# Performance work log

Hardware: AMD Instinct MI355X
Metric: run time of the kernel (lower is better)

## Reference

```python
import jax, jax.numpy as jnp
import numpy as np

_PHI = (1.0 + 5.0 ** 0.5) / 2.0
_VS = np.array([[0, 1, _PHI], [0, 1, -_PHI], [0, -1, _PHI], [0, -1, -_PHI],
                [1, _PHI, 0], [1, -_PHI, 0], [-1, _PHI, 0], [-1, -_PHI, 0],
                [_PHI, 0, 1], [_PHI, 0, -1], [-_PHI, 0, 1], [-_PHI, 0, -1]], dtype=np.float32)
_VS = _VS / np.linalg.norm(_VS, axis=-1, keepdims=True)  # 12 icosahedron vertices
_COLOR_COM = np.array([(0, 1, 2, 3, 4, 5), (0, 5, 4, 3, 2, 1), (2, 5, 4, 1, 0, 3), (5, 0, 1, 3, 2, 4),
                       (3, 5, 2, 0, 4, 1), (4, 0, 5, 2, 1, 3), (1, 3, 4, 2, 0, 5), (1, 0, 2, 4, 3, 5),
                       (4, 1, 2, 5, 0, 3), (3, 1, 4, 0, 2, 5), (5, 1, 0, 4, 2, 3), (2, 4, 5, 3, 0, 1)])
_INV = np.argsort(_COLOR_COM, axis=-1)  # inverse perms: scatter_(-1, color_com, W) == gather with _INV
_C2V = np.array([(0, 1), (6, 7), (2, 11), (4, 9), (5, 8), (3, 10)])
_ROLL = np.array([(0, 1, 2, 3, 4, 5), (0, 2, 3, 4, 5, 1), (0, 3, 4, 5, 1, 2), (0, 4, 5, 1, 2, 3), (0, 5, 1, 2, 3, 4)])
_HEADS = 8


def _build_sym(Wp):
    """(..., 18) raw params -> (..., 13, 12, 6) symmetry-expanded weights."""
    lead = Wp.shape[:-1]
    top = jnp.concatenate([Wp[..., 0:1], jnp.repeat(Wp[..., 1:2], 5, axis=-1)], axis=-1)[..., None, :]
    bot = jnp.concatenate([Wp[..., 2:3], jnp.repeat(Wp[..., 3:4], 5, axis=-1)], axis=-1)[..., None, :]
    cen = jnp.concatenate([Wp[..., 4:5], jnp.repeat(Wp[..., 5:6], 5, axis=-1)], axis=-1)[..., None, :]
    sym = Wp[..., 6:18].reshape(lead + (2, 6))[..., _ROLL].reshape(lead + (10, 6))
    W13 = jnp.concatenate([top, bot, sym, cen], axis=-2)  # (..., 13, 6)
    return W13[..., _INV]  # (..., 13, 12, 6): rotated copies via inverse color permutations


def setup_inputs() -> dict:
    key = jax.random.key(0)
    ks = jax.random.split(key, 6)
    bs, V, n, di, do = 1, 2048, 16, 32, 64
    s = 0.05
    return {
        "neighbor_index": jax.random.randint(ks[0], (bs, V, n), 0, V),
        "vertices": jax.random.normal(ks[1], (bs, V, 3), dtype=jnp.float32),
        "feature_map": jax.random.normal(ks[2], (bs, di, V, 6), dtype=jnp.float32),
        "W_dim": jax.random.normal(ks[3], (di + 1, di), dtype=jnp.float32) * s,
        "W": jax.random.normal(ks[4], (do, di, 18), dtype=jnp.float32) * s,
        "W_dir": jax.random.normal(ks[5], (di * _HEADS, 18), dtype=jnp.float32) * s,
    }


def reference(neighbor_index, vertices, feature_map, W_dim, W, W_dir):
    bs, V, n = neighbor_index.shape
    do, di, _ = W.shape
    H = _HEADS
    dph = di // H
    vs = jnp.asarray(_VS)
    c2v = jnp.asarray(_C2V)
    # neighbor direction (normalized)
    neigh = jax.vmap(lambda v, idx: v[idx])(vertices, neighbor_index)  # (bs,V,n,3)
    nd = neigh - vertices[:, :, None, :]
    ndn = nd / jnp.maximum(jnp.linalg.norm(nd, axis=-1, keepdims=True), 1e-12)
    # symmetry-expanded weights
    W_ro = _build_sym(W)       # (do, di, 13, 12, 6)
    Wd_ro = _build_sym(W_dir)  # (di*H, 13, 12, 6)
    # gather neighbor features: (bs, di, V, n, 6)
    nf = jax.vmap(lambda fm, idx: fm[:, idx])(feature_map, neighbor_index)
    # direction features discretized onto the 6 color axes
    de = jnp.einsum('vi,bqni->bqnv', vs, ndn)          # (bs,V,n,12)
    de = de[..., c2v].max(axis=-1)                      # (bs,V,n,6)
    cross = jnp.concatenate([nf, de[:, None]], axis=1)  # (bs, di+1, V, n, 6)
    cross = jnp.einsum('co,bcpni->bopni', W_dim, cross)  # (bs, di, V, n, 6)
    # per-head attention over neighbors
    Wdr = Wd_ro.reshape(H, di, 13, 12, 6).transpose(0, 1, 2, 4, 3)  # (h, c, k, i, r)
    act = jnp.einsum('hckir,bcpni->hbkpnr', Wdr[:, :, :12], cross) / (dph ** 0.5)
    act = jax.nn.softmax(act, axis=-2)                  # softmax over neighbors n
    cross_h = cross.reshape(bs, H, dph, V, n, 6)
    nfm = jnp.einsum('hbkpnr,bhcpni->bhckpir', act, cross_h).reshape(bs, di, 12, V, 6, 12)
    feat = jnp.einsum('dckri,bckpir->bdkpr', W_ro[:, :, :12], nfm)   # (bs,do,12,V,12)
    center = jnp.einsum('dcri,bcpi->bdpr', W_ro[:, :, 12], feature_map)  # (bs,do,V,12)
    ka = feat.sum(axis=2) + center                       # (bs,do,V,12)
    ka = ka[..., c2v].max(axis=-1)                       # (bs,do,V,6)
    return (ka, feature_map)
```

## Files before the change

kernel.cpp:

```cpp
#include <hip/hip_runtime.h>
#include <cstdint>
#include <cstddef>

#define NN 16
#define DI 32
#define DO 64

typedef short bf16x8 __attribute__((ext_vector_type(8)));
typedef short bf16x4 __attribute__((ext_vector_type(4)));
typedef float f32x4 __attribute__((ext_vector_type(4)));

#if defined(__has_builtin)
#  if __has_builtin(__builtin_amdgcn_mfma_f32_16x16x16_bf16)
#    define MFMA_K16(a, b, c) __builtin_amdgcn_mfma_f32_16x16x16_bf16(a, b, c, 0, 0, 0)
#    define HAVE_K16 1
#  elif __has_builtin(__builtin_amdgcn_mfma_f32_16x16x16bf16_1k)
#    define MFMA_K16(a, b, c) __builtin_amdgcn_mfma_f32_16x16x16bf16_1k(a, b, c, 0, 0, 0)
#    define HAVE_K16 1
#  endif
#  if __has_builtin(__builtin_amdgcn_cvt_pk_bf16_f32)
#    define HAVE_PKBF 1
#  endif
#endif

__device__ __constant__ int c_INV[12][6] = {
  {0,1,2,3,4,5},{0,5,4,3,2,1},{4,3,0,5,2,1},{1,2,4,3,5,0},
  {3,5,2,0,4,1},{1,4,3,5,0,2},{4,0,3,1,2,5},{1,0,2,4,3,5},
  {4,1,2,5,0,3},{3,1,4,0,2,5},{2,1,4,5,3,0},{4,5,0,3,1,2}};
__device__ __constant__ int c_ROLL[5][6] = {
  {0,1,2,3,4,5},{0,2,3,4,5,1},{0,3,4,5,1,2},{0,4,5,1,2,3},{0,5,1,2,3,4}};
__device__ __constant__ float c_VS[12][3] = {
  {0.f, 0.5257311121f, 0.8506508084f},
  {0.f, 0.5257311121f, -0.8506508084f},
  {0.f, -0.5257311121f, 0.8506508084f},
  {0.f, -0.5257311121f, -0.8506508084f},
  {0.5257311121f, 0.8506508084f, 0.f},
  {0.5257311121f, -0.8506508084f, 0.f},
  {-0.5257311121f, 0.8506508084f, 0.f},
  {-0.5257311121f, -0.8506508084f, 0.f},
  {0.8506508084f, 0.f, 0.5257311121f},
  {0.8506508084f, 0.f, -0.5257311121f},
  {-0.8506508084f, 0.f, 0.5257311121f},
  {-0.8506508084f, 0.f, -0.5257311121f}};
__device__ __constant__ int c_C2V[6][2] = {{0,1},{6,7},{2,11},{4,9},{5,8},{3,10}};

__device__ inline unsigned short f2bf(float f) {
  unsigned int u = __float_as_uint(f);
  unsigned int r = (u + 0x7fffu + ((u >> 16) & 1u)) >> 16;
  return (unsigned short)r;
}
__device__ inline unsigned int pk2(float a, float b) {
#ifdef HAVE_PKBF
  typedef __bf16 bf16v2 __attribute__((ext_vector_type(2)));
  union { bf16v2 v; unsigned int u; } cv;
  cv.v = __builtin_amdgcn_cvt_pk_bf16_f32(a, b);
  return cv.u;
#else
  return (unsigned int)f2bf(a) | ((unsigned int)f2bf(b) << 16);
#endif
}
__device__ inline unsigned short f2bf_fast(float a) {
  return (unsigned short)(pk2(a, a) & 0xffffu);
}

__device__ inline float sym13(const float* __restrict__ w, int k, int j) {
  if (k == 0)  return w[j == 0 ? 0 : 1];
  if (k == 1)  return w[j == 0 ? 2 : 3];
  if (k == 12) return w[j == 0 ? 4 : 5];
  int a = (k - 2) / 5, rr = (k - 2) % 5;
  return w[6 + a * 6 + c_ROLL[rr][j]];
}

__global__ __launch_bounds__(256) void k0_expand(
    const float* __restrict__ W, const float* __restrict__ Wdir,
    const float* __restrict__ fm, const float* __restrict__ Wdim,
    unsigned short* __restrict__ A_bf,
    unsigned short* __restrict__ W2k,
    unsigned short* __restrict__ Wck,
    unsigned short* __restrict__ fmTbf,
    unsigned short* __restrict__ wdB,
    float* __restrict__ out_fm, int V) {
  int idx = blockIdx.x * 256 + threadIdx.x;
  if (idx < 221184) {
    int row = idx / 192, ci = idx % 192;
    int h = row / 144, k = (row / 12) % 12, r = row % 12;
    int c = ci / 6, i = ci % 6;
    int rt = row >> 4, rl = row & 15;
    int ks = ci >> 5, q = (ci >> 3) & 3, j = ci & 7;
    A_bf[(((rt * 6 + ks) * 4 + q) * 16 + rl) * 8 + j] =
        f2bf_fast(0.5f * sym13(&Wdir[(h * 32 + c) * 18], k, c_INV[r][i]));
  } else if (idx < 1990656) {
    int e = idx - 221184;
    int kr = e / 12288, rem = e % 12288;
    int k = kr / 12, r = kr % 12, d = rem / 192, ci = rem % 192;
    int c = ci / 6, i = ci % 6;
    int ks = ci >> 5, q = (ci >> 3) & 3, j = ci & 7;
    W2k[kr * 12288 + ((ks * 4 + q) * 64 + d) * 8 + j] =
        f2bf_fast(sym13(&W[(d * 32 + c) * 18], k, c_INV[r][i]));
  } else if (idx < 2138112) {
    int e = idx - 1990656;
    int r = e / 12288, rem = e % 12288, d = rem / 192, ci = rem % 192;
    int c = ci / 6, i = ci % 6;
    int ks = ci >> 5, q = (ci >> 3) & 3, j = ci & 7;
    Wck[r * 12288 + ((ks * 4 + q) * 64 + d) * 8 + j] =
        f2bf_fast(sym13(&W[(d * 32 + c) * 18], 12, c_INV[r][i]));
  } else if (idx < 2138112 + 192 * V) {
    int e = idx - 2138112;
    int p = e / 192, ci = e % 192, c = ci / 6, i = ci % 6;
    float v = fm[(c * V + p) * 6 + i];
    fmTbf[e] = f2bf_fast(v);
    out_fm[(c * V + p) * 6 + i] = v;
  } else {
    int e = idx - (2138112 + 192 * V);
    if (e < 2048) {
      int j = e & 7, lane = (e >> 3) & 63, kc = (e >> 9) & 1, ot = e >> 10;
      int k = kc * 32 + (lane >> 4) * 8 + j;
      int o = ot * 16 + (lane & 15);
      wdB[e] = (k <= 32) ? f2bf_fast(Wdim[k * 32 + o]) : (unsigned short)0;
    }
  }
}

__global__ __launch_bounds__(256) void k1_cross(
    const int* __restrict__ nbi, const float* __restrict__ verts,
    const float* __restrict__ fm, const unsigned short* __restrict__ wdB,
    unsigned short* __restrict__ cross_n,
    unsigned short* __restrict__ crossT_g, int V) {
  __shared__ __align__(16) unsigned short in_bf[4][96][64];
  int t = threadIdx.x, w = t >> 6, lane = t & 63;
  int quad = lane >> 4, col = lane & 15;
  int p = blockIdx.x * 4 + w;
  unsigned short* mybuf = &in_bf[w][0][0];

  for (int z = lane; z < 384; z += 64) {
    int m = z >> 2, q = z & 3;
    *(uint4*)&mybuf[m * 64 + 32 + q * 8] = make_uint4(0u, 0u, 0u, 0u);
  }

  float px = verts[p * 3 + 0], py = verts[p * 3 + 1], pz = verts[p * 3 + 2];
  for (int idx = lane; idx < 528; idx += 64) {
    int n = idx / 33, c = idx - n * 33;
    int nb = nbi[p * 16 + n];
    if (c < 32) {
      const float* src = fm + ((size_t)c * V + nb) * 6;
      float2 a  = *(const float2*)(src + 0);
      float2 b  = *(const float2*)(src + 2);
      float2 cd = *(const float2*)(src + 4);
      unsigned short* dst = &mybuf[(n * 6) * 64 + c];
      dst[0 * 64] = f2bf_fast(a.x);
      dst[1 * 64] = f2bf_fast(a.y);
      dst[2 * 64] = f2bf_fast(b.x);
      dst[3 * 64] = f2bf_fast(b.y);
      dst[4 * 64] = f2bf_fast(cd.x);
      dst[5 * 64] = f2bf_fast(cd.y);
    } else {
      float qx = verts[nb * 3 + 0] - px;
      float qy = verts[nb * 3 + 1] - py;
      float qz = verts[nb * 3 + 2] - pz;
      float L = sqrtf(qx * qx + qy * qy + qz * qz);
      float inv = 1.0f / fmaxf(L, 1e-12f);
      qx *= inv; qy *= inv; qz *= inv;
      float de[12];
      #pragma unroll
      for (int v = 0; v < 12; ++v)
        de[v] = c_VS[v][0] * qx + c_VS[v][1] * qy + c_VS[v][2] * qz;
      #pragma unroll
      for (int j = 0; j < 6; ++j)
        mybuf[(n * 6 + j) * 64 + 32] = f2bf_fast(fmaxf(de[c_C2V[j][0]], de[c_C2V[j][1]]));
    }
  }

  bf16x8 Bf[2][2];
  #pragma unroll
  for (int ot = 0; ot < 2; ++ot)
    #pragma unroll
    for (int kc = 0; kc < 2; ++kc)
      Bf[ot][kc] = *(const bf16x8*)(wdB + (size_t)((ot * 2 + kc) * 64 + lane) * 8);

  asm volatile("s_waitcnt lgkmcnt(0)" ::: "memory");

  f32x4 D[6][2];
  #pragma unroll
  for (int mt = 0; mt < 6; ++mt) {
    bf16x8 a0 = *(const bf16x8*)&mybuf[(mt * 16 + col) * 64 + quad * 8];
    bf16x8 a1 = *(const bf16x8*)&mybuf[(mt * 16 + col) * 64 + 32 + quad * 8];
    #pragma unroll
    for (int ot = 0; ot < 2; ++ot) {
      f32x4 acc = (f32x4){0.f, 0.f, 0.f, 0.f};
      acc = __builtin_amdgcn_mfma_f32_16x16x32_bf16(a0, Bf[ot][0], acc, 0, 0, 0);
      acc = __builtin_amdgcn_mfma_f32_16x16x32_bf16(a1, Bf[ot][1], acc, 0, 0, 0);
      D[mt][ot] = acc;
    }
  }

  asm volatile("s_waitcnt lgkmcnt(0)" ::: "memory");
  unsigned short* crossL = mybuf;
  #pragma unroll
  for (int mt = 0; mt < 6; ++mt) {
    #pragma unroll
    for (int ot = 0; ot < 2; ++ot) {
      #pragma unroll
      for (int r = 0; r < 4; ++r) {
        int m = mt * 16 + quad * 4 + r;
        int n = m / 6, i = m - n * 6;
        int ci = (ot * 16 + col) * 6 + i;
        crossL[ci * 16 + n] = f2bf_fast(D[mt][ot][r]);
      }
    }
  }
  asm volatile("s_waitcnt lgkmcnt(0)" ::: "memory");

  {
    uint4* ct = (uint4*)(crossT_g + (size_t)p * 3072);
    const uint4* cl4 = (const uint4*)crossL;
    for (int q = lane; q < 384; q += 64) ct[q] = cl4[q];
  }
  {
    uint4* cn = (uint4*)(cross_n + (size_t)p * 3072);
    for (int q = lane; q < 384; q += 64) {
      int n = (q * 8) / 192, ci0 = (q * 8) % 192;
      unsigned int u[4];
      #pragma unroll
      for (int h2 = 0; h2 < 4; ++h2) {
        unsigned int lo = crossL[(ci0 + 2 * h2 + 0) * 16 + n];
        unsigned int hi = crossL[(ci0 + 2 * h2 + 1) * 16 + n];
        u[h2] = lo | (hi << 16);
      }
      cn[q] = make_uint4(u[0], u[1], u[2], u[3]);
    }
  }
}

__global__ __launch_bounds__(512, 4) void k2_main(
    const unsigned short* __restrict__ A_bf,
    const unsigned short* __restrict__ cross_n,
    const unsigned short* __restrict__ crossT_g,
    unsigned short* __restrict__ nfm, int V) {
#ifdef HAVE_K16
  __shared__ __align__(16) unsigned short crossT[4][192][16];
#else
  __shared__ __align__(16) unsigned short crossT[4][192][40];
#endif
  int t = threadIdx.x;
  int w = t >> 6, lane = t & 63;
  int quad = lane >> 4, col = lane & 15;
  int p0 = blockIdx.x * 4;
  int pw = w & 1, tw = w >> 1;

  bf16x8 Afr[2][6];
  #pragma unroll
  for (int pi = 0; pi < 2; ++pi)
    #pragma unroll
    for (int ks = 0; ks < 6; ++ks)
      Afr[pi][ks] = *(const bf16x8*)(cross_n + (size_t)(p0 + pw * 2 + pi) * 3072 +
                                     col * 192 + ks * 32 + quad * 8);

#ifdef HAVE_K16
  for (int idx = t; idx < 1536; idx += 512) {
    *(uint4*)&((unsigned short*)crossT)[idx * 8] =
        *(const uint4*)(crossT_g + (size_t)p0 * 3072 + idx * 8);
  }
#else
  for (int idx = t; idx < 1536; idx += 512) {
    int p = idx / 384, rem = idx % 384, ci = rem >> 1, half = rem & 1;
    *(uint4*)&crossT[p][ci][half * 8] =
        *(const uint4*)(crossT_g + (size_t)(p0 + p) * 3072 + ci * 16 + half * 8);
  }
  for (int idx = t; idx < 1536; idx += 512) {
    int p = idx / 384, rem = idx % 384, ci = rem >> 1, half = rem & 1;
    *(uint4*)&crossT[p][ci][16 + half * 8] = make_uint4(0u, 0u, 0u, 0u);
  }
#endif
  __syncthreads();

#ifndef HAVE_K16
  int s0l = quad * 32 + col;
  int s1l = s0l + 16;
#endif

  for (int rt = tw; rt < 72; rt += 4) {
    int h = rt / 9;
    f32x4 acc[2];
    acc[0] = (f32x4){0.f, 0.f, 0.f, 0.f};
    acc[1] = (f32x4){0.f, 0.f, 0.f, 0.f};
    const unsigned short* Abase = A_bf + rt * 3072 + quad * 128 + col * 8;
    #pragma unroll
    for (int ks = 0; ks < 6; ++ks) {
      bf16x8 wf = *(const bf16x8*)(Abase + ks * 512);
      acc[0] = __builtin_amdgcn_mfma_f32_16x16x32_bf16(Afr[0][ks], wf, acc[0], 0, 0, 0);
      acc[1] = __builtin_amdgcn_mfma_f32_16x16x32_bf16(Afr[1][ks], wf, acc[1], 0, 0, 0);
    }
    int row0 = h * 24 + col;
    int row1 = min(h * 24 + 16 + col, 191);
    #pragma unroll
    for (int pi = 0; pi < 2; ++pi) {
      int p_i = pw * 2 + pi;
      float v0 = acc[pi][0], v1 = acc[pi][1], v2 = acc[pi][2], v3 = acc[pi][3];
      float mx = fmaxf(fmaxf(v0, v1), fmaxf(v2, v3));
      mx = fmaxf(mx, __shfl_xor(mx, 16));
      mx = fmaxf(mx, __shfl_xor(mx, 32));
      float e0 = __expf(v0 - mx), e1 = __expf(v1 - mx);
      float e2 = __expf(v2 - mx), e3 = __expf(v3 - mx);
      float s = (e0 + e1) + (e2 + e3);
      s += __shfl_xor(s, 16);
      s += __shfl_xor(s, 32);
      float inv = __builtin_amdgcn_rcpf(s);
      unsigned int lo = pk2(e0 * inv, e1 * inv);
      unsigned int hi = pk2(e2 * inv, e3 * inv);
      f32x4 o0 = (f32x4){0.f, 0.f, 0.f, 0.f}, o1 = o0;
#ifdef HAVE_K16
      union { uint2 u; bf16x4 v; } bcvt;
      bcvt.u = make_uint2(lo, hi);
      bf16x4 a0 = *(const bf16x4*)&crossT[p_i][row0][quad * 4];
      bf16x4 a1 = *(const bf16x4*)&crossT[p_i][row1][quad * 4];
      o0 = MFMA_K16(a0, bcvt.v, o0);
      o1 = MFMA_K16(a1, bcvt.v, o1);
#else
      unsigned int b0 = (unsigned int)__shfl((int)lo, s0l);
      unsigned int b1 = (unsigned int)__shfl((int)hi, s0l);
      unsigned int b2 = (unsigned int)__shfl((int)lo, s1l);
      unsigned int b3 = (unsigned int)__shfl((int)hi, s1l);
      bool vq = (quad < 2);
      union { uint4 u; bf16x8 v; } cvt;
      cvt.u = make_uint4(vq ? b0 : 0u, vq ? b1 : 0u, vq ? b2 : 0u, vq ? b3 : 0u);
      bf16x8 a0 = *(const bf16x8*)&crossT[p_i][row0][quad * 8];
      bf16x8 a1 = *(const bf16x8*)&crossT[p_i][row1][quad * 8];
      o0 = __builtin_amdgcn_mfma_f32_16x16x32_bf16(a0, cvt.v, o0, 0, 0, 0);
      o1 = __builtin_amdgcn_mfma_f32_16x16x32_bf16(a1, cvt.v, o1, 0, 0, 0);
#endif
      size_t rowbase = (size_t)blockIdx.x * 110592 + (size_t)(rt * 16 + col) * 96 + p_i * 24;
      uint2 w0;
      w0.x = pk2(o0[0], o0[1]);
      w0.y = pk2(o0[2], o0[3]);
      *(uint2*)(nfm + rowbase + quad * 4) = w0;
      if (quad < 2) {
        uint2 w1;
        w1.x = pk2(o1[0], o1[1]);
        w1.y = pk2(o1[2], o1[3]);
        *(uint2*)(nfm + rowbase + 16 + quad * 4) = w1;
      }
    }
  }
}

__global__ __launch_bounds__(512) void k3_feat(
    const unsigned short* __restrict__ W2k,
    const unsigned short* __restrict__ Wck,
    const unsigned short* __restrict__ fmTbf,
    const unsigned short* __restrict__ nfm,
    float* __restrict__ out, int V) {
  __shared__ float red[2][3][32][64];
  int pb = blockIdx.x, j = blockIdx.y;
  int t = threadIdx.x, w = t >> 6, lane = t & 63;
  int rhalf = w >> 2, kw = w & 3;
  int r = c_C2V[j][rhalf];
  int quad = lane >> 4, col = lane & 15;
  int p0 = pb * 32;
  f32x4 acc[4][2];
  #pragma unroll
  for (int m = 0; m < 4; ++m)
    #pragma unroll
    for (int jj = 0; jj < 2; ++jj) acc[m][jj] = (f32x4){0.f, 0.f, 0.f, 0.f};

  int base24[6];
  #pragma unroll
  for (int ks = 0; ks < 6; ++ks) {
    int ci = ks * 32 + quad * 8;
    int hh = ci / 24, oo = ci - hh * 24;
    base24[ks] = hh * 13824 + oo;
  }

  int pA = p0 + col, pB = p0 + 16 + col;
  const unsigned short* Bn0 = nfm + (size_t)(pA >> 2) * 110592 + (pA & 3) * 24;
  const unsigned short* Bn1 = nfm + (size_t)(pB >> 2) * 110592 + (pB & 3) * 24;
  const unsigned short* Bc0 = fmTbf + (size_t)pA * 192;
  const unsigned short* Bc1 = fmTbf + (size_t)pB * 192;

  int nkb = (kw == 3) ? 4 : 3;
  for (int i = 0; i < nkb; ++i) {
    int kb = kw * 3 + i;
    const unsigned short* Ab;
    int kr96 = 0;
    if (kb < 12) { Ab = W2k + (size_t)(kb * 12 + r) * 12288; kr96 = (kb * 12 + r) * 96; }
    else         { Ab = Wck + (size_t)r * 12288; }
    const unsigned short* Albase = Ab + quad * 512 + col * 8;
    #pragma unroll
    for (int ks = 0; ks < 6; ++ks) {
      bf16x8 b0, b1;
      if (kb < 12) {
        b0 = *(const bf16x8*)(Bn0 + base24[ks] + kr96);
        b1 = *(const bf16x8*)(Bn1 + base24[ks] + kr96);
      } else {
        int ko = ks * 32 + quad * 8;
        b0 = *(const bf16x8*)(Bc0 + ko);
        b1 = *(const bf16x8*)(Bc1 + ko);
      }
      #pragma unroll
      for (int m = 0; m < 4; ++m) {
        bf16x8 a = *(const bf16x8*)(Albase + ks * 2048 + m * 128);
        acc[m][0] = __builtin_amdgcn_mfma_f32_16x16x32_bf16(a, b0, acc[m][0], 0, 0, 0);
        acc[m][1] = __builtin_amdgcn_mfma_f32_16x16x32_bf16(a, b1, acc[m][1], 0, 0, 0);
      }
    }
  }
  if (kw > 0) {
    #pragma unroll
    for (int m = 0; m < 4; ++m)
      #pragma unroll
      for (int jj = 0; jj < 2; ++jj)
        #pragma unroll
        for (int rr = 0; rr < 4; ++rr)
          red[rhalf][kw - 1][m * 8 + jj * 4 + rr][lane] = acc[m][jj][rr];
  }
  __syncthreads();
  if (kw == 0) {
    #pragma unroll
    for (int m = 0; m < 4; ++m)
      #pragma unroll
      for (int jj = 0; jj < 2; ++jj)
        #pragma unroll
        for (int rr = 0; rr < 4; ++rr) {
          int ri = m * 8 + jj * 4 + rr;
          acc[m][jj][rr] += red[rhalf][0][ri][lane] + red[rhalf][1][ri][lane] + red[rhalf][2][ri][lane];
        }
  }
  if (w == 4) {
    #pragma unroll
    for (int m = 0; m < 4; ++m)
      #pragma unroll
      for (int jj = 0; jj < 2; ++jj)
        #pragma unroll
        for (int rr = 0; rr < 4; ++rr)
          red[1][0][m * 8 + jj * 4 + rr][lane] = acc[m][jj][rr];
  }
  __syncthreads();
  if (w == 0) {
    #pragma unroll
    for (int m = 0; m < 4; ++m)
      #pragma unroll
      for (int jj = 0; jj < 2; ++jj)
        #pragma unroll
        for (int rr = 0; rr < 4; ++rr) {
          float v = fmaxf(acc[m][jj][rr], red[1][0][m * 8 + jj * 4 + rr][lane]);
          int d = m * 16 + quad * 4 + rr;
          int p = p0 + jj * 16 + col;
          out[((size_t)d * V + p) * 6 + j] = v;
        }
  }
}

extern "C" void kernel_launch(void* const* d_in, const int* in_sizes, int n_in,
                              void* d_out, int out_size, void* d_ws, size_t ws_size,
                              hipStream_t stream) {
  const int* nbi = (const int*)d_in[0];
  const float* verts = (const float*)d_in[1];
  const float* fm = (const float*)d_in[2];
  const float* Wdim = (const float*)d_in[3];
  const float* W = (const float*)d_in[4];
  const float* Wdir = (const float*)d_in[5];
  float* out = (float*)d_out;
  float* ws = (float*)d_ws;
  int V = in_sizes[0] / NN;

  unsigned short* A_bf  = (unsigned short*)ws;
  unsigned short* W2k   = (unsigned short*)(ws + 110592);
  unsigned short* Wck   = (unsigned short*)(ws + 995328);
  unsigned short* fmTbf = (unsigned short*)(ws + 1069056);
  size_t o = 1069056 + (size_t)96 * V;
  unsigned short* cross_n = (unsigned short*)(ws + o);
  o += (size_t)1536 * V;
  unsigned short* crossT_g = (unsigned short*)(ws + o);
  o += (size_t)1536 * V;
  unsigned short* nfm = (unsigned short*)(ws + o);
  o += (size_t)13824 * V;
  unsigned short* wdB = (unsigned short*)(ws + o);

  int n0 = 2138112 + 192 * V + 2048;
  k0_expand<<<(n0 + 255) / 256, 256, 0, stream>>>(W, Wdir, fm, Wdim, A_bf, W2k, Wck, fmTbf,
                                                  wdB, out + (size_t)DO * V * 6, V);
  k1_cross<<<V / 4, 256, 0, stream>>>(nbi, verts, fm, wdB, cross_n, crossT_g, V);
  k2_main<<<V / 4, 512, 0, stream>>>(A_bf, cross_n, crossT_g, nfm, V);
  k3_feat<<<dim3(V / 32, 6), 512, 0, stream>>>(W2k, Wck, fmTbf, nfm, out, V);
}
```

Before: 178.7 us.

## Fuse cross-feature and attention kernels, keeping cross tile in shared memory

Merges the cross-feature kernel and the attention kernel into one launch. Each 256-thread block now handles 2 vertices, and the cross tile stays in LDS, so the cross_n and crossT global round trips go away. The direction feature term is added as a scalar FMA in fp32 instead of being padded into a second K=32 MFMA, which halves the Wdim fragment. In exchange, only 2 of the 4 waves do the cross MFMA while the rest idle. Fragments are gathered element by element from LDS, and the nfm layout changes to 2 vertices per block.

```diff
diff --git a/kernel.cpp b/kernel.cpp
--- a/kernel.cpp
+++ b/kernel.cpp
@@ -112,173 +112,114 @@
     out_fm[(c * V + p) * 6 + i] = v;
   } else {
     int e = idx - (2138112 + 192 * V);
-    if (e < 2048) {
-      int j = e & 7, lane = (e >> 3) & 63, kc = (e >> 9) & 1, ot = e >> 10;
-      int k = kc * 32 + (lane >> 4) * 8 + j;
+    if (e < 1024) {
+      int j = e & 7, lane = (e >> 3) & 63, ot = e >> 9;
+      int k = ((lane >> 4) & 3) * 8 + j;
       int o = ot * 16 + (lane & 15);
-      wdB[e] = (k <= 32) ? f2bf_fast(Wdim[k * 32 + o]) : (unsigned short)0;
-    }
-  }
-}
-
-__global__ __launch_bounds__(256) void k1_cross(
+      wdB[e] = f2bf_fast(Wdim[k * 32 + o]);
+    }
+  }
+}
+
+__global__ __launch_bounds__(256, 4) void k12_main(
     const int* __restrict__ nbi, const float* __restrict__ verts,
-    const float* __restrict__ fm, const unsigned short* __restrict__ wdB,
-    unsigned short* __restrict__ cross_n,
-    unsigned short* __restrict__ crossT_g, int V) {
-  __shared__ __align__(16) unsigned short in_bf[4][96][64];
-  int t = threadIdx.x, w = t >> 6, lane = t & 63;
-  int quad = lane >> 4, col = lane & 15;
-  int p = blockIdx.x * 4 + w;
-  unsigned short* mybuf = &in_bf[w][0][0];
-
-  for (int z = lane; z < 384; z += 64) {
-    int m = z >> 2, q = z & 3;
-    *(uint4*)&mybuf[m * 64 + 32 + q * 8] = make_uint4(0u, 0u, 0u, 0u);
-  }
-
-  float px = verts[p * 3 + 0], py = verts[p * 3 + 1], pz = verts[p * 3 + 2];
-  for (int idx = lane; idx < 528; idx += 64) {
-    int n = idx / 33, c = idx - n * 33;
-    int nb = nbi[p * 16 + n];
-    if (c < 32) {
-      const float* src = fm + ((size_t)c * V + nb) * 6;
-      float2 a  = *(const float2*)(src + 0);
-      float2 b  = *(const float2*)(src + 2);
-      float2 cd = *(const float2*)(src + 4);
-      unsigned short* dst = &mybuf[(n * 6) * 64 + c];
-      dst[0 * 64] = f2bf_fast(a.x);
-      dst[1 * 64] = f2bf_fast(a.y);
-      dst[2 * 64] = f2bf_fast(b.x);
-      dst[3 * 64] = f2bf_fast(b.y);
-      dst[4 * 64] = f2bf_fast(cd.x);
-      dst[5 * 64] = f2bf_fast(cd.y);
-    } else {
-      float qx = verts[nb * 3 + 0] - px;
-      float qy = verts[nb * 3 + 1] - py;
-      float qz = verts[nb * 3 + 2] - pz;
-      float L = sqrtf(qx * qx + qy * qy + qz * qz);
-      float inv = 1.0f / fmaxf(L, 1e-12f);
-      qx *= inv; qy *= inv; qz *= inv;
-      float de[12];
-      #pragma unroll
-      for (int v = 0; v < 12; ++v)
-        de[v] = c_VS[v][0] * qx + c_VS[v][1] * qy + c_VS[v][2] * qz;
-      #pragma unroll
-      for (int j = 0; j < 6; ++j)
-        mybuf[(n * 6 + j) * 64 + 32] = f2bf_fast(fmaxf(de[c_C2V[j][0]], de[c_C2V[j][1]]));
-    }
-  }
-
-  bf16x8 Bf[2][2];
-  #pragma unroll
-  for (int ot = 0; ot < 2; ++ot)
-    #pragma unroll
-    for (int kc = 0; kc < 2; ++kc)
-      Bf[ot][kc] = *(const bf16x8*)(wdB + (size_t)((ot * 2 + kc) * 64 + lane) * 8);
-
-  asm volatile("s_waitcnt lgkmcnt(0)" ::: "memory");
-
-  f32x4 D[6][2];
-  #pragma unroll
-  for (int mt = 0; mt < 6; ++mt) {
-    bf16x8 a0 = *(const bf16x8*)&mybuf[(mt * 16 + col) * 64 + quad * 8];
-    bf16x8 a1 = *(const bf16x8*)&mybuf[(mt * 16 + col) * 64 + 32 + quad * 8];
-    #pragma unroll
-    for (int ot = 0; ot < 2; ++ot) {
-      f32x4 acc = (f32x4){0.f, 0.f, 0.f, 0.f};
-      acc = __builtin_amdgcn_mfma_f32_16x16x32_bf16(a0, Bf[ot][0], acc, 0, 0, 0);
-      acc = __builtin_amdgcn_mfma_f32_16x16x32_bf16(a1, Bf[ot][1], acc, 0, 0, 0);
-      D[mt][ot] = acc;
-    }
-  }
-
-  asm volatile("s_waitcnt lgkmcnt(0)" ::: "memory");
-  unsigned short* crossL = mybuf;
-  #pragma unroll
-  for (int mt = 0; mt < 6; ++mt) {
-    #pragma unroll
-    for (int ot = 0; ot < 2; ++ot) {
-      #pragma unroll
-      for (int r = 0; r < 4; ++r) {
-        int m = mt * 16 + quad * 4 + r;
-        int n = m / 6, i = m - n * 6;
-        int ci = (ot * 16 + col) * 6 + i;
-        crossL[ci * 16 + n] = f2bf_fast(D[mt][ot][r]);
-      }
-    }
-  }
-  asm volatile("s_waitcnt lgkmcnt(0)" ::: "memory");
-
-  {
-    uint4* ct = (uint4*)(crossT_g + (size_t)p * 3072);
-    const uint4* cl4 = (const uint4*)crossL;
-    for (int q = lane; q < 384; q += 64) ct[q] = cl4[q];
-  }
-  {
-    uint4* cn = (uint4*)(cross_n + (size_t)p * 3072);
-    for (int q = lane; q < 384; q += 64) {
-      int n = (q * 8) / 192, ci0 = (q * 8) % 192;
-      unsigned int u[4];
-      #pragma unroll
-      for (int h2 = 0; h2 < 4; ++h2) {
-        unsigned int lo = crossL[(ci0 + 2 * h2 + 0) * 16 + n];
-        unsigned int hi = crossL[(ci0 + 2 * h2 + 1) * 16 + n];
-        u[h2] = lo | (hi << 16);
-      }
-      cn[q] = make_uint4(u[0], u[1], u[2], u[3]);
-    }
-  }
-}
-
-__global__ __launch_bounds__(512, 4) void k2_main(
+    const float* __restrict__ fm, const float* __restrict__ Wdim,
+    const unsigned short* __restrict__ wdB,
     const unsigned short* __restrict__ A_bf,
-    const unsigned short* __restrict__ cross_n,
-    const unsigned short* __restrict__ crossT_g,
     unsigned short* __restrict__ nfm, int V) {
-#ifdef HAVE_K16
-  __shared__ __align__(16) unsigned short crossT[4][192][16];
-#else
-  __shared__ __align__(16) unsigned short crossT[4][192][40];
-#endif
+  __shared__ __align__(16) unsigned short in_bf[2][96][40];
+  __shared__ __align__(16) float de_s[2][96];
+  __shared__ __align__(16) unsigned short crossL[2][192][20];
   int t = threadIdx.x;
   int w = t >> 6, lane = t & 63;
   int quad = lane >> 4, col = lane & 15;
-  int p0 = blockIdx.x * 4;
-  int pw = w & 1, tw = w >> 1;
+  int p0 = blockIdx.x * 2;
+  int v = w & 1, hf = w >> 1;
+  int p = p0 + v;
+
+  for (int i = lane; i < 256; i += 64) {
+    int n = i >> 4, c = hf * 16 + (i & 15);
+    int nb = nbi[p * 16 + n];
+    const float* src = fm + ((size_t)c * V + nb) * 6;
+    float2 a  = *(const float2*)(src + 0);
+    float2 b  = *(const float2*)(src + 2);
+    float2 cd = *(const float2*)(src + 4);
+    unsigned short* dst = &in_bf[v][n * 6][c];
+    dst[0 * 40] = f2bf_fast(a.x);
+    dst[1 * 40] = f2bf_fast(a.y);
+    dst[2 * 40] = f2bf_fast(b.x);
+    dst[3 * 40] = f2bf_fast(b.y);
+    dst[4 * 40] = f2bf_fast(cd.x);
+    dst[5 * 40] = f2bf_fast(cd.y);
+  }
+  if (hf == 0 && lane < 16) {
+    int n = lane, nb = nbi[p * 16 + n];
+    float px = verts[p * 3 + 0], py = verts[p * 3 + 1], pz = verts[p * 3 + 2];
+    float qx = verts[nb * 3 + 0] - px, qy = verts[nb * 3 + 1] - py, qz = verts[nb * 3 + 2] - pz;
+    float L = sqrtf(qx * qx + qy * qy + qz * qz);
+    float inv = 1.0f / fmaxf(L, 1e-12f);
+    qx *= inv; qy *= inv; qz *= inv;
+    float de[12];
+    #pragma unroll
+    for (int vv = 0; vv < 12; ++vv)
+      de[vv] = c_VS[vv][0] * qx + c_VS[vv][1] * qy + c_VS[vv][2] * qz;
+    #pragma unroll
+    for (int j = 0; j < 6; ++j)
+      de_s[v][n * 6 + j] = fmaxf(de[c_C2V[j][0]], de[c_C2V[j][1]]);
+  }
+  __syncthreads();
+
+  if (w < 2) {
+    int vv = w;
+    bf16x8 Bf[2];
+    #pragma unroll
+    for (int ot = 0; ot < 2; ++ot)
+      Bf[ot] = *(const bf16x8*)(wdB + (size_t)(ot * 64 + lane) * 8);
+    float wd32[2] = {Wdim[1024 + col], Wdim[1024 + 16 + col]};
+    f32x4 D[6][2];
+    #pragma unroll
+    for (int mt = 0; mt < 6; ++mt) {
+      bf16x8 a0 = *(const bf16x8*)&in_bf[vv][mt * 16 + col][quad * 8];
+      f32x4 du = *(const f32x4*)&de_s[vv][mt * 16 + quad * 4];
+      #pragma unroll
+      for (int ot = 0; ot < 2; ++ot) {
+        f32x4 acc = (f32x4){0.f, 0.f, 0.f, 0.f};
+        acc = __builtin_amdgcn_mfma_f32_16x16x32_bf16(a0, Bf[ot], acc, 0, 0, 0);
+        #pragma unroll
+        for (int r = 0; r < 4; ++r)
+          acc[r] = fmaf(du[r], wd32[ot], acc[r]);
+        D[mt][ot] = acc;
+      }
+    }
+    #pragma unroll
+    for (int mt = 0; mt < 6; ++mt) {
+      #pragma unroll
+      for (int ot = 0; ot < 2; ++ot) {
+        #pragma unroll
+        for (int r = 0; r < 4; ++r) {
+          int m = mt * 16 + quad * 4 + r;
+          int n = m / 6, i = m - n * 6;
+          crossL[vv][(ot * 16 + col) * 6 + i][n] = f2bf_fast(D[mt][ot][r]);
+        }
+      }
+    }
+  }
+  __syncthreads();
 
   bf16x8 Afr[2][6];
   #pragma unroll
-  for (int pi = 0; pi < 2; ++pi)
-    #pragma unroll
-    for (int ks = 0; ks < 6; ++ks)
-      Afr[pi][ks] = *(const bf16x8*)(cross_n + (size_t)(p0 + pw * 2 + pi) * 3072 +
-                                     col * 192 + ks * 32 + quad * 8);
-
-#ifdef HAVE_K16
-  for (int idx = t; idx < 1536; idx += 512) {
-    *(uint4*)&((unsigned short*)crossT)[idx * 8] =
-        *(const uint4*)(crossT_g + (size_t)p0 * 3072 + idx * 8);
-  }
-#else
-  for (int idx = t; idx < 1536; idx += 512) {
-    int p = idx / 384, rem = idx % 384, ci = rem >> 1, half = rem & 1;
-    *(uint4*)&crossT[p][ci][half * 8] =
-        *(const uint4*)(crossT_g + (size_t)(p0 + p) * 3072 + ci * 16 + half * 8);
-  }
-  for (int idx = t; idx < 1536; idx += 512) {
-    int p = idx / 384, rem = idx % 384, ci = rem >> 1, half = rem & 1;
-    *(uint4*)&crossT[p][ci][16 + half * 8] = make_uint4(0u, 0u, 0u, 0u);
-  }
-#endif
-  __syncthreads();
-
-#ifndef HAVE_K16
-  int s0l = quad * 32 + col;
-  int s1l = s0l + 16;
-#endif
-
-  for (int rt = tw; rt < 72; rt += 4) {
+  for (int pi = 0; pi < 2; ++pi) {
+    #pragma unroll
+    for (int ks = 0; ks < 6; ++ks) {
+      union { unsigned short s[8]; bf16x8 v8; } u;
+      #pragma unroll
+      for (int j = 0; j < 8; ++j)
+        u.s[j] = crossL[pi][ks * 32 + quad * 8 + j][col];
+      Afr[pi][ks] = u.v8;
+    }
+  }
+
+  for (int rt = w; rt < 72; rt += 4) {
     int h = rt / 9;
     f32x4 acc[2];
     acc[0] = (f32x4){0.f, 0.f, 0.f, 0.f};
@@ -294,7 +235,6 @@
     int row1 = min(h * 24 + 16 + col, 191);
     #pragma unroll
     for (int pi = 0; pi < 2; ++pi) {
-      int p_i = pw * 2 + pi;
       float v0 = acc[pi][0], v1 = acc[pi][1], v2 = acc[pi][2], v3 = acc[pi][3];
       float mx = fmaxf(fmaxf(v0, v1), fmaxf(v2, v3));
       mx = fmaxf(mx, __shfl_xor(mx, 16));
@@ -309,26 +249,32 @@
       unsigned int hi = pk2(e2 * inv, e3 * inv);
       f32x4 o0 = (f32x4){0.f, 0.f, 0.f, 0.f}, o1 = o0;
 #ifdef HAVE_K16
-      union { uint2 u; bf16x4 v; } bcvt;
+      union { uint2 u; bf16x4 v4; } bcvt;
       bcvt.u = make_uint2(lo, hi);
-      bf16x4 a0 = *(const bf16x4*)&crossT[p_i][row0][quad * 4];
-      bf16x4 a1 = *(const bf16x4*)&crossT[p_i][row1][quad * 4];
-      o0 = MFMA_K16(a0, bcvt.v, o0);
-      o1 = MFMA_K16(a1, bcvt.v, o1);
+      bf16x4 a0 = *(const bf16x4*)&crossL[pi][row0][quad * 4];
+      bf16x4 a1 = *(const bf16x4*)&crossL[pi][row1][quad * 4];
+      o0 = MFMA_K16(a0, bcvt.v4, o0);
+      o1 = MFMA_K16(a1, bcvt.v4, o1);
 #else
+      int s0l = quad * 32 + col, s1l = s0l + 16;
       unsigned int b0 = (unsigned int)__shfl((int)lo, s0l);
       unsigned int b1 = (unsigned int)__shfl((int)hi, s0l);
       unsigned int b2 = (unsigned int)__shfl((int)lo, s1l);
       unsigned int b3 = (unsigned int)__shfl((int)hi, s1l);
       bool vq = (quad < 2);
-      union { uint4 u; bf16x8 v; } cvt;
+      union { uint4 u; bf16x8 v8; } cvt;
       cvt.u = make_uint4(vq ? b0 : 0u, vq ? b1 : 0u, vq ? b2 : 0u, vq ? b3 : 0u);
-      bf16x8 a0 = *(const bf16x8*)&crossT[p_i][row0][quad * 8];
-      bf16x8 a1 = *(const bf16x8*)&crossT[p_i][row1][quad * 8];
-      o0 = __builtin_amdgcn_mfma_f32_16x16x32_bf16(a0, cvt.v, o0, 0, 0, 0);
-      o1 = __builtin_amdgcn_mfma_f32_16x16x32_bf16(a1, cvt.v, o1, 0, 0, 0);
+      union { unsigned short s[8]; bf16x8 v8; } ua0, ua1;
+      #pragma unroll
+      for (int j = 0; j < 8; ++j) {
+        int nn = quad * 8 + j;
+        ua0.s[j] = (nn < 16) ? crossL[pi][row0][nn] : (unsigned short)0;
+        ua1.s[j] = (nn < 16) ? crossL[pi][row1][nn] : (unsigned short)0;
+      }
+      o0 = __builtin_amdgcn_mfma_f32_16x16x32_bf16(ua0.v8, cvt.v8, o0, 0, 0, 0);
+      o1 = __builtin_amdgcn_mfma_f32_16x16x32_bf16(ua1.v8, cvt.v8, o1, 0, 0, 0);
 #endif
-      size_t rowbase = (size_t)blockIdx.x * 110592 + (size_t)(rt * 16 + col) * 96 + p_i * 24;
+      size_t rowbase = (size_t)blockIdx.x * 55296 + (size_t)(rt * 16 + col) * 48 + pi * 24;
       uint2 w0;
       w0.x = pk2(o0[0], o0[1]);
       w0.y = pk2(o0[2], o0[3]);
@@ -367,12 +313,12 @@
   for (int ks = 0; ks < 6; ++ks) {
     int ci = ks * 32 + quad * 8;
     int hh = ci / 24, oo = ci - hh * 24;
-    base24[ks] = hh * 13824 + oo;
+    base24[ks] = hh * 6912 + oo;
   }
 
   int pA = p0 + col, pB = p0 + 16 + col;
-  const unsigned short* Bn0 = nfm + (size_t)(pA >> 2) * 110592 + (pA & 3) * 24;
-  const unsigned short* Bn1 = nfm + (size_t)(pB >> 2) * 110592 + (pB & 3) * 24;
+  const unsigned short* Bn0 = nfm + (size_t)(pA >> 1) * 55296 + (pA & 1) * 24;
+  const unsigned short* Bn1 = nfm + (size_t)(pB >> 1) * 55296 + (pB & 1) * 24;
   const unsigned short* Bc0 = fmTbf + (size_t)pA * 192;
   const unsigned short* Bc1 = fmTbf + (size_t)pB * 192;
 
@@ -380,16 +326,16 @@
   for (int i = 0; i < nkb; ++i) {
     int kb = kw * 3 + i;
     const unsigned short* Ab;
-    int kr96 = 0;
-    if (kb < 12) { Ab = W2k + (size_t)(kb * 12 + r) * 12288; kr96 = (kb * 12 + r) * 96; }
+    int kr48 = 0;
+    if (kb < 12) { Ab = W2k + (size_t)(kb * 12 + r) * 12288; kr48 = (kb * 12 + r) * 48; }
     else         { Ab = Wck + (size_t)r * 12288; }
     const unsigned short* Albase = Ab + quad * 512 + col * 8;
     #pragma unroll
     for (int ks = 0; ks < 6; ++ks) {
       bf16x8 b0, b1;
       if (kb < 12) {
-        b0 = *(const bf16x8*)(Bn0 + base24[ks] + kr96);
-        b1 = *(const bf16x8*)(Bn1 + base24[ks] + kr96);
+        b0 = *(const bf16x8*)(Bn0 + base24[ks] + kr48);
+        b1 = *(const bf16x8*)(Bn1 + base24[ks] + kr48);
       } else {
         int ko = ks * 32 + quad * 8;
         b0 = *(const bf16x8*)(Bc0 + ko);
@@ -467,18 +413,13 @@
   unsigned short* Wck   = (unsigned short*)(ws + 995328);
   unsigned short* fmTbf = (unsigned short*)(ws + 1069056);
   size_t o = 1069056 + (size_t)96 * V;
-  unsigned short* cross_n = (unsigned short*)(ws + o);
-  o += (size_t)1536 * V;
-  unsigned short* crossT_g = (unsigned short*)(ws + o);
-  o += (size_t)1536 * V;
   unsigned short* nfm = (unsigned short*)(ws + o);
   o += (size_t)13824 * V;
   unsigned short* wdB = (unsigned short*)(ws + o);
 
-  int n0 = 2138112 + 192 * V + 2048;
+  int n0 = 2138112 + 192 * V + 1024;
   k0_expand<<<(n0 + 255) / 256, 256, 0, stream>>>(W, Wdir, fm, Wdim, A_bf, W2k, Wck, fmTbf,
                                                   wdB, out + (size_t)DO * V * 6, V);
-  k1_cross<<<V / 4, 256, 0, stream>>>(nbi, verts, fm, wdB, cross_n, crossT_g, V);
-  k2_main<<<V / 4, 512, 0, stream>>>(A_bf, cross_n, crossT_g, nfm, V);
+  k12_main<<<V / 2, 256, 0, stream>>>(nbi, verts, fm, Wdim, wdB, A_bf, nfm, V);
   k3_feat<<<dim3(V / 32, 6), 512, 0, stream>>>(W2k, Wck, fmTbf, nfm, out, V);
 }
```

Result: faster. 158.1 us (-11.5%).
